# Performance work log

Measured on AMD Instinct MI355X. Metric: run time of the kernel, lower is better.

The kernel has to match this reference:

```python
import jax, jax.numpy as jnp
from jax import lax
import numpy as np

B = 16384
D = 32
N_HEADS = 4


def _piece_table():
    base = np.zeros((7, 4, 4), np.int32)
    cells = [
        [(1, 0), (1, 1), (1, 2), (1, 3)],  # I
        [(1, 1), (1, 2), (2, 1), (2, 2)],  # O
        [(1, 1), (2, 0), (2, 1), (2, 2)],  # T
        [(1, 1), (1, 2), (2, 0), (2, 1)],  # S
        [(1, 0), (1, 1), (2, 1), (2, 2)],  # Z
        [(1, 0), (2, 0), (2, 1), (2, 2)],  # J
        [(1, 2), (2, 0), (2, 1), (2, 2)],  # L
    ]
    for i, cs in enumerate(cells):
        for (r, c) in cs:
            base[i, r, c] = 1
    rots = np.stack([np.stack([np.rot90(base[i], k) for k in range(4)]) for i in range(7)])
    p = np.concatenate([rots, np.zeros((1, 4, 4, 4), np.int32)], 0)  # [8,4,4,4]
    return jnp.asarray(p)


def setup_inputs() -> dict:
    key = jax.random.key(0)
    ks = jax.random.split(key, 24)

    def ri(k, n, lo, hi):
        return jax.random.randint(k, (B, n), lo, hi, dtype=jnp.int32)

    t = jnp.concatenate([
        ri(ks[0], 1, 0, 10),   # col0 feature
        ri(ks[1], 1, 2, 8),
        ri(ks[2], 1, 0, 10),   # col2 y pos
        ri(ks[3], 1, 0, 8),    # col3 drop dist
        ri(ks[4], 1, 0, 4),    # col4 rotation
        ri(ks[5], 3, 0, 10),   # cols5-7
        ri(ks[6], 1, 0, 7),    # col8 piece id
        ri(ks[7], 6, 0, 7),    # cols9-14 hold/next
        ri(ks[8], 7, 0, 10),   # cols15-21
        ri(ks[9], 210, 0, 2),  # cols22-231 board
    ], axis=1)

    s = 0.05
    rn = lambda k, shp: jax.random.normal(k, shp, jnp.float32) * s
    return {
        "t": t,
        "piece_table": _piece_table(),
        "conv1_w": rn(ks[10], (6, 3, 5, 5)), "conv1_b": rn(ks[11], (6,)),
        "conv2_w": rn(ks[12], (16, 6, 5, 5)), "conv2_b": rn(ks[13], (16,)),
        "conv3_w": rn(ks[14], (64, 16, 3, 1)), "conv3_b": rn(ks[15], (64,)),
        "lfc1_w": rn(ks[16], (32, 64)), "lfc1_b": rn(ks[17], (32,)),
        "fc_w": rn(ks[18], (32, 8)), "fc_b": rn(ks[19], (32,)),
        "emb": rn(ks[20], (8, D)),
        "in_proj_w": rn(ks[21], (3 * D, D)), "in_proj_b": jnp.zeros((3 * D,), jnp.float32),
        "out_proj_w": rn(ks[22], (D, D)), "out_proj_b": jnp.zeros((D,), jnp.float32),
    }


def _avgpool2(x):
    b, c, h, w = x.shape
    h2, w2 = h // 2, w // 2
    return x[:, :, :h2 * 2, :w2 * 2].reshape(b, c, h2, 2, w2, 2).mean((3, 5))


def _lenet(x, w1, b1, w2, b2, w3, b3, fw, fb):
    dn = ("NCHW", "OIHW", "NCHW")
    x = jax.nn.relu(lax.conv_general_dilated(x, w1, (1, 1), ((2, 2), (2, 2)), dimension_numbers=dn) + b1[None, :, None, None])
    x = _avgpool2(x)                                   # [B,6,11,6]
    x = jax.nn.relu(lax.conv_general_dilated(x, w2, (1, 1), ((0, 0), (0, 0)), dimension_numbers=dn) + b2[None, :, None, None])
    x = _avgpool2(x)                                   # [B,16,3,1]
    x = jax.nn.relu(lax.conv_general_dilated(x, w3, (1, 1), ((0, 0), (0, 0)), dimension_numbers=dn) + b3[None, :, None, None])
    x = x.reshape(-1, 64)
    return jax.nn.relu(x @ fw.T + fb)                  # [B,32]


def _pe():
    pos = jnp.array([0, 0, 1, 2, 3, 4, 5], jnp.float32)[:, None]
    div = jnp.exp(jnp.arange(0, D, 2, dtype=jnp.float32) * (-jnp.log(10000.0) / D))
    s, c = jnp.sin(pos * div), jnp.cos(pos * div)      # [7,16] each
    return jnp.stack([s, c], -1).reshape(7, D)         # interleaved sin/cos


def _mha(q_in, kv, in_w, in_b, out_w, out_b):
    qw, kw, vw = in_w[:D], in_w[D:2 * D], in_w[2 * D:]
    qb, kb, vb = in_b[:D], in_b[D:2 * D], in_b[2 * D:]
    b, lq, _ = q_in.shape
    hd = D // N_HEADS
    q = (q_in @ qw.T + qb).reshape(b, lq, N_HEADS, hd)
    k = (kv @ kw.T + kb).reshape(b, -1, N_HEADS, hd)
    v = (kv @ vw.T + vb).reshape(b, -1, N_HEADS, hd)
    scores = jnp.einsum("bqhd,bkhd->bhqk", q, k) / jnp.sqrt(jnp.float32(hd))
    w = jax.nn.softmax(scores, axis=-1)
    o = jnp.einsum("bhqk,bkhd->bqhd", w, v).reshape(b, lq, D)
    return o @ out_w.T + out_b


def reference(t, piece_table, conv1_w, conv1_b, conv2_w, conv2_b, conv3_w, conv3_b,
              lfc1_w, lfc1_b, fc_w, fc_b, emb, in_proj_w, in_proj_b, out_proj_w, out_proj_b):
    bsz = t.shape[0]
    board = jnp.zeros((bsz, 3, 21, 10), jnp.float32)
    board = board.at[:, 0].set(t[:, 22:232].astype(jnp.float32).reshape(bsz, 21, 10))

    # gather piece grid, extract the 4 filled cells per sample in row-major order
    pieces = piece_table[t[:, 8], t[:, 4]].reshape(bsz, 16)        # [B,16] in {0,1}
    idx = jnp.argsort(1 - pieces, axis=1, stable=True)[:, :4]      # first 4 ones, scan order
    cy, cx = idx // 4, idx % 4
    x = cx + t[:, 1][:, None] - 2
    y = cy + t[:, 2][:, None]
    ny = y + t[:, 3][:, None]
    mask = (y >= 0) & (ny >= 0)
    br = jnp.arange(bsz, dtype=jnp.int32)[:, None]
    y_m = jnp.where(mask, y, -1)
    ny_m = jnp.where(mask, ny, -1)
    board = board.at[br, 1, y_m, x].set(1.0, mode="drop")
    board = board.at[br, 2, ny_m, x].set(1.0, mode="drop")

    board = jnp.pad(board, ((0, 0), (0, 0), (0, 1), (1, 1)), constant_values=1.0)  # [B,3,22,12]

    t9 = jnp.where((t[:, 9] != -1) & (t[:, 6] != 0), t[:, 9], 7)
    hold_next = jnp.concatenate([t[:, 8:9], t9[:, None], t[:, 10:15]], axis=1)     # [B,7]

    b2 = _lenet(board, conv1_w, conv1_b, conv2_w, conv2_b, conv3_w, conv3_b, lfc1_w, lfc1_b)  # [B,32]
    bkv = b2[:, None, :]                                            # [B,1,32]
    p = emb[hold_next] + _pe()[None]                                # [B,7,32]
    a = _mha(p, bkv, in_proj_w, in_proj_b, out_proj_w, out_proj_b)  # [B,7,32]

    xf = jax.nn.relu(t[:, :8].astype(jnp.float32) @ fc_w.T + fc_b)  # [B,32]
    out = jnp.concatenate([xf, a.mean(axis=1), b2], axis=1)         # [B,96]
    return (out, board)
```

## Files before the change

### kernel.cpp

```cpp
#include <hip/hip_runtime.h>
#include <cstddef>


#define BATCH 16384
#define SPB   4
#define NBLK  (BATCH / SPB)
#define RS    18
#define SBE_SZ 432
#define P1OFF  432
#define PCSOFF 800
#define SS2    816

__global__ __launch_bounds__(256)
void cborder_kernel(const float* __restrict__ w1, float* __restrict__ cb)
{
  int i = blockIdx.x * 256 + threadIdx.x;
  if (i >= 1584) return;
  int p = i / 6, o = i - p * 6;
  int y0 = p / 12, x0 = p - y0 * 12;
  float acc = 0.f;
#pragma unroll
  for (int dy = 0; dy < 5; ++dy)
#pragma unroll
    for (int dx = 0; dx < 5; ++dx) {
      int pr = y0 + dy - 2, pc = x0 + dx - 2;
      if (pr >= 0 && pr < 22 && pc >= 0 && pc < 12 &&
          (pr == 21 || pc == 0 || pc == 11)) {
        int k = dy * 5 + dx;
        acc += w1[(o * 3 + 0) * 25 + k] + w1[(o * 3 + 1) * 25 + k]
             + w1[(o * 3 + 2) * 25 + k];
      }
    }
  cb[p * 6 + o] = acc;
}

__global__ __launch_bounds__(256)
void board_model_kernel(const int* __restrict__ t,
                        const int* __restrict__ piece_table,
                        const float* __restrict__ w1, const float* __restrict__ b1,
                        const float* __restrict__ w2, const float* __restrict__ b2w,
                        const float* __restrict__ w3, const float* __restrict__ b3,
                        const float* __restrict__ wf1, const float* __restrict__ bf1,
                        const float* __restrict__ fcw, const float* __restrict__ fcb,
                        const float* __restrict__ ipw, const float* __restrict__ ipb,
                        const float* __restrict__ opw, const float* __restrict__ opb,
                        const float* __restrict__ cbg,
                        float* __restrict__ out,
                        float* __restrict__ out_board)
{
  __shared__ __align__(16) float scr[SPB * SS2];
  __shared__ float w1L[300];
  __shared__ float cbL[1440];

  const int tid  = threadIdx.x;
  const int lane = tid & 63;
  const int wv   = tid >> 6;
  const int bb   = blockIdx.x * SPB;

  for (int i = tid; i < 300; i += 256)
    w1L[i] = w1[(i / 50) * 75 + 25 + (i % 50)];
  for (int i = tid; i < 1440; i += 256) cbL[i] = cbg[i];

  {
    float* W = &scr[wv * SS2];
    int*   pcs = (int*)&scr[wv * SS2 + PCSOFF];
    const int* tr = t + (size_t)(bb + wv) * 232;

    float4* W4 = (float4*)W;
    for (int i = lane; i < 108; i += 64) W4[i] = float4{0.f, 0.f, 0.f, 0.f};

    for (int i = lane; i < 210; i += 64) {
      int r = i / 10, b = i - r * 10;
      W[(r + 2) * RS + b + 5] = (float)tr[22 + i];
    }

    if (lane < 4) {
      const int* pt = piece_table + (tr[8] * 4 + tr[4]) * 16;
      int sel = -1, n1 = 0;
#pragma unroll
      for (int j = 0; j < 16; ++j) { if (pt[j]) { if (n1 == lane) sel = j; ++n1; } }
      if (sel < 0) {
        int n0 = 0, want = lane - n1;
#pragma unroll
        for (int j = 0; j < 16; ++j) if (!pt[j]) { if (n0 == want) { sel = j; break; } ++n0; }
      }
      int cy = sel >> 2, cx = sel & 3;
      int x  = cx + tr[1] - 2;
      int y  = cy + tr[2];
      int ny = y + tr[3];
      bool mask = (y >= 0) && (ny >= 0);
      bool xok  = (x >= 0) && (x < 10);
      bool v1 = mask && xok && (y < 21);
      bool v2 = mask && xok && (ny < 21);
      pcs[2 * lane + 0]       = v1 ? y  : -100;
      pcs[2 * lane + 1]       = x + 1;
      pcs[2 * (lane + 4)]     = v2 ? ny : -100;
      pcs[2 * (lane + 4) + 1] = x + 1;
    }
    __builtin_amdgcn_wave_barrier();

    float* ob = out_board + (size_t)(bb + wv) * 792;
    for (int v = lane; v < 198; v += 64) {
      int j0 = v * 4;
      int ch = j0 / 264, rem = j0 - ch * 264;
      int r = rem / 12, c = rem - r * 12;
      float val[4];
      if (ch == 0) {
#pragma unroll
        for (int d = 0; d < 4; ++d) {
          int cd = c + d;
          val[d] = (r == 21 || cd == 0 || cd == 11) ? 1.f
                 : W[(r + 2) * RS + cd + 4];
        }
      } else {
#pragma unroll
        for (int d = 0; d < 4; ++d) {
          int cd = c + d;
          val[d] = (r == 21 || cd == 0 || cd == 11) ? 1.f : 0.f;
        }
#pragma unroll
        for (int e = 0; e < 4; ++e) {
          int pr = pcs[2 * ((ch - 1) * 4 + e)];
          int pc = pcs[2 * ((ch - 1) * 4 + e) + 1];
          if (pr == r && (unsigned)(pc - c) < 4u) val[pc - c] = 1.f;
        }
      }
      *(float4*)(ob + j0) = float4{val[0], val[1], val[2], val[3]};
    }
  }
  __syncthreads();

  if (lane < 60) {
    int p = lane;
    int r = p / 6, c = p - r * 6;
    const float* Wq  = &scr[wv * SS2];
    const int*   pcs = (const int*)&scr[wv * SS2 + PCSOFF];
    float acc[2][2][6];
#pragma unroll
    for (int i = 0; i < 2; ++i)
#pragma unroll
      for (int j = 0; j < 2; ++j) {
        int pcell = (2 * r + i) * 12 + (2 * c + j);
#pragma unroll
        for (int o = 0; o < 6; ++o)
          acc[i][j][o] = b1[o] + cbL[pcell * 6 + o];
      }

    {
      const float* base = Wq + (2 * r) * RS + (2 * c + 2);
#pragma unroll
      for (int u = 0; u < 6; ++u) {
        float2 a0 = *(const float2*)(base + u * RS);
        float2 a1 = *(const float2*)(base + u * RS + 2);
        float2 a2 = *(const float2*)(base + u * RS + 4);
        float rv[6] = {a0.x, a0.y, a1.x, a1.y, a2.x, a2.y};
#pragma unroll
        for (int i = 0; i < 2; ++i) {
          if (u - i < 0 || u - i > 4) continue;
          const int ky = u - i;
#pragma unroll
          for (int j = 0; j < 2; ++j)
#pragma unroll
            for (int kx = 0; kx < 5; ++kx) {
              float xv = rv[j + kx];
#pragma unroll
              for (int o = 0; o < 6; ++o)
                acc[i][j][o] += xv * w1[o * 75 + ky * 5 + kx];
            }
        }
      }
    }

#pragma unroll
    for (int e = 0; e < 8; ++e) {
      int pr = pcs[2 * e];
      if (pr < 0) continue;
      int pc = pcs[2 * e + 1];
      int chm = e >> 2;
      int dyb = pr + 2 - 2 * r;
      int dxb = pc + 2 - 2 * c;
      if (dyb < 0 || dyb > 5 || dxb < 0 || dxb > 5) continue;
#pragma unroll
      for (int i = 0; i < 2; ++i) {
        int dy = dyb - i;
        if ((unsigned)dy >= 5u) continue;
#pragma unroll
        for (int j = 0; j < 2; ++j) {
          int dx = dxb - j;
          if ((unsigned)dx >= 5u) continue;
#pragma unroll
          for (int o = 0; o < 6; ++o)
            acc[i][j][o] += w1L[(o * 2 + chm) * 25 + dy * 5 + dx];
        }
      }
    }

    float* P1q = &scr[wv * SS2 + P1OFF];
#pragma unroll
    for (int o = 0; o < 6; ++o) {
      float v = fmaxf(acc[0][0][o], 0.f) + fmaxf(acc[0][1][o], 0.f)
              + fmaxf(acc[1][0][o], 0.f) + fmaxf(acc[1][1][o], 0.f);
      P1q[o * 61 + p] = 0.25f * v;
    }
  }
  __syncthreads();

  const int wvu = __builtin_amdgcn_readfirstlane(wv);

  if (lane < 48) {
    int q = lane / 12, p = lane - q * 12;
    int r = p >> 1, c = p & 1;
    const float* P1q = &scr[q * SS2 + P1OFF];
    float a4[4];
#pragma unroll
    for (int oo = 0; oo < 4; ++oo) a4[oo] = b2w[4 * wvu + oo];
    for (int ic = 0; ic < 6; ++ic)
#pragma unroll
      for (int kr = 0; kr < 5; ++kr) {
        float xv[5];
#pragma unroll
        for (int kc = 0; kc < 5; ++kc)
          xv[kc] = P1q[ic * 61 + (r + kr) * 6 + c + kc];
#pragma unroll
        for (int kc = 0; kc < 5; ++kc)
#pragma unroll
          for (int oo = 0; oo < 4; ++oo)
            a4[oo] += xv[kc] * w2[(((4 * wvu + oo) * 6 + ic) * 5 + kr) * 5 + kc];
      }
    float* C2q = &scr[q * SS2];
#pragma unroll
    for (int oo = 0; oo < 4; ++oo)
      C2q[(4 * wvu + oo) * 12 + p] = fmaxf(a4[oo], 0.f);
  }
  __syncthreads();

  {
    const int q = wvu;
    float* S = &scr[q * SS2];

    if (lane < 48) {
      int o = lane / 3, pr = lane - o * 3;
      float v = 0.25f * (S[o * 12 + 4 * pr] + S[o * 12 + 4 * pr + 1]
                       + S[o * 12 + 4 * pr + 2] + S[o * 12 + 4 * pr + 3]);
      S[192 + lane] = v;
    }
    __builtin_amdgcn_wave_barrier();

    {
      int o = lane;
      float acc = b3[o];
#pragma unroll
      for (int k = 0; k < 48; ++k) acc += S[192 + k] * w3[o * 48 + k];
      S[240 + o] = fmaxf(acc, 0.f);
    }
    __builtin_amdgcn_wave_barrier();

    {
      int j = lane & 31, h = lane >> 5;
      float part = 0.f;
#pragma unroll
      for (int kk = 0; kk < 32; ++kk) {
        int k = 32 * h + kk;
        part += S[240 + k] * wf1[j * 64 + k];
      }
      part += __shfl_xor(part, 32, 64);
      if (h == 0) {
        float acc = fmaxf(bf1[j] + part, 0.f);
        S[304 + j] = acc;
        out[(size_t)(bb + q) * 96 + 64 + j] = acc;
      }
    }
    __builtin_amdgcn_wave_barrier();

    {
      int j = lane & 31;
      if (lane < 32) {
        float acc = ipb[64 + j];
#pragma unroll
        for (int k = 0; k < 32; ++k) acc += S[304 + k] * ipw[(64 + j) * 32 + k];
        S[336 + j] = acc;
      } else {
        const int* tr = t + (size_t)(bb + q) * 232;
        float acc = fcb[j];
#pragma unroll
        for (int k = 0; k < 8; ++k) acc += (float)tr[k] * fcw[j * 8 + k];
        out[(size_t)(bb + q) * 96 + j] = fmaxf(acc, 0.f);
      }
    }
    __builtin_amdgcn_wave_barrier();

    if (lane < 32) {
      int j = lane;
      float acc = opb[j];
#pragma unroll
      for (int k = 0; k < 32; ++k) acc += S[336 + k] * opw[j * 32 + k];
      out[(size_t)(bb + q) * 96 + 32 + j] = acc;
    }
  }
}

extern "C" void kernel_launch(void* const* d_in, const int* in_sizes, int n_in,
                              void* d_out, int out_size, void* d_ws, size_t ws_size,
                              hipStream_t stream) {
  const int*   t   = (const int*)d_in[0];
  const int*   pt  = (const int*)d_in[1];
  const float* w1  = (const float*)d_in[2];
  const float* b1  = (const float*)d_in[3];
  const float* w2  = (const float*)d_in[4];
  const float* b2w = (const float*)d_in[5];
  const float* w3  = (const float*)d_in[6];
  const float* b3  = (const float*)d_in[7];
  const float* wf1 = (const float*)d_in[8];
  const float* bf1 = (const float*)d_in[9];
  const float* fcw = (const float*)d_in[10];
  const float* fcb = (const float*)d_in[11];
  const float* ipw = (const float*)d_in[13];
  const float* ipb = (const float*)d_in[14];
  const float* opw = (const float*)d_in[15];
  const float* opb = (const float*)d_in[16];

  float* out       = (float*)d_out;
  float* out_board = out + (size_t)BATCH * 96;
  float* cbg       = (float*)d_ws;

  hipLaunchKernelGGL(cborder_kernel, dim3(7), dim3(256), 0, stream, w1, cbg);
  hipLaunchKernelGGL(board_model_kernel, dim3(NBLK), dim3(256), 0, stream,
                     t, pt, w1, b1, w2, b2w, w3, b3, wf1, bf1, fcw, fcb,
                     ipw, ipb, opw, opb, cbg, out, out_board);
}
```

Measured before the change: 196.3 us.

## Make each wave independent, drop block barriers, and repartition conv2 per wave

Every block-wide __syncthreads is replaced by wave-local fences and barriers, so each wave processes its own sample with no cross-wave dependency. conv2 is reassigned so each wave computes all 16 output channels for its own sample: 4 lanes per channel, 3 output rows each, with per-channel weights held in registers. The w1L shared staging is removed and the piece-cell conv1 terms now read w1 from global memory. Each wave also loads the whole cbL table itself, which adds redundant global traffic. The small dense layers use packed two-wide float vectors to encourage packed FMA instructions.

Result: slower. 219.5 us (+11.8%).

```diff
diff --git a/kernel.cpp b/kernel.cpp
--- a/kernel.cpp
+++ b/kernel.cpp
@@ -1,12 +1,13 @@
 #include <hip/hip_runtime.h>
 #include <cstddef>
 
+
+typedef float f32x2 __attribute__((ext_vector_type(2)));
 
 #define BATCH 16384
 #define SPB   4
 #define NBLK  (BATCH / SPB)
 #define RS    18
-#define SBE_SZ 432
 #define P1OFF  432
 #define PCSOFF 800
 #define SS2    816
@@ -31,7 +32,7 @@
              + w1[(o * 3 + 2) * 25 + k];
       }
     }
-  cb[p * 6 + o] = acc;
+  cb[i] = acc;
 }
 
 __global__ __launch_bounds__(256)
@@ -49,23 +50,20 @@
                         float* __restrict__ out_board)
 {
   __shared__ __align__(16) float scr[SPB * SS2];
-  __shared__ float w1L[300];
   __shared__ float cbL[1440];
 
   const int tid  = threadIdx.x;
   const int lane = tid & 63;
   const int wv   = tid >> 6;
-  const int bb   = blockIdx.x * SPB;
-
-  for (int i = tid; i < 300; i += 256)
-    w1L[i] = w1[(i / 50) * 75 + 25 + (i % 50)];
-  for (int i = tid; i < 1440; i += 256) cbL[i] = cbg[i];
+  const int s    = blockIdx.x * SPB + wv;
+
+  float* W   = &scr[wv * SS2];
+  int*   pcs = (int*)&scr[wv * SS2 + PCSOFF];
+  const int* tr = t + (size_t)s * 232;
+
+  for (int i = lane; i < 1440; i += 64) cbL[i] = cbg[i];
 
   {
-    float* W = &scr[wv * SS2];
-    int*   pcs = (int*)&scr[wv * SS2 + PCSOFF];
-    const int* tr = t + (size_t)(bb + wv) * 232;
-
     float4* W4 = (float4*)W;
     for (int i = lane; i < 108; i += 64) W4[i] = float4{0.f, 0.f, 0.f, 0.f};
 
@@ -97,9 +95,12 @@
       pcs[2 * (lane + 4)]     = v2 ? ny : -100;
       pcs[2 * (lane + 4) + 1] = x + 1;
     }
-    __builtin_amdgcn_wave_barrier();
-
-    float* ob = out_board + (size_t)(bb + wv) * 792;
+  }
+  __threadfence_block();
+  __builtin_amdgcn_wave_barrier();
+
+  {
+    float* ob = out_board + (size_t)s * 792;
     for (int v = lane; v < 198; v += 64) {
       int j0 = v * 4;
       int ch = j0 / 264, rem = j0 - ch * 264;
@@ -128,13 +129,10 @@
       *(float4*)(ob + j0) = float4{val[0], val[1], val[2], val[3]};
     }
   }
-  __syncthreads();
 
   if (lane < 60) {
     int p = lane;
     int r = p / 6, c = p - r * 6;
-    const float* Wq  = &scr[wv * SS2];
-    const int*   pcs = (const int*)&scr[wv * SS2 + PCSOFF];
     float acc[2][2][6];
 #pragma unroll
     for (int i = 0; i < 2; ++i)
@@ -147,7 +145,7 @@
       }
 
     {
-      const float* base = Wq + (2 * r) * RS + (2 * c + 2);
+      const float* base = W + (2 * r) * RS + (2 * c + 2);
 #pragma unroll
       for (int u = 0; u < 6; ++u) {
         float2 a0 = *(const float2*)(base + u * RS);
@@ -190,12 +188,12 @@
           if ((unsigned)dx >= 5u) continue;
 #pragma unroll
           for (int o = 0; o < 6; ++o)
-            acc[i][j][o] += w1L[(o * 2 + chm) * 25 + dy * 5 + dx];
-        }
-      }
-    }
-
-    float* P1q = &scr[wv * SS2 + P1OFF];
+            acc[i][j][o] += w1[(o * 3 + 1 + chm) * 25 + dy * 5 + dx];
+        }
+      }
+    }
+
+    float* P1q = W + P1OFF;
 #pragma unroll
     for (int o = 0; o < 6; ++o) {
       float v = fmaxf(acc[0][0][o], 0.f) + fmaxf(acc[0][1][o], 0.f)
@@ -203,40 +201,51 @@
       P1q[o * 61 + p] = 0.25f * v;
     }
   }
-  __syncthreads();
-
-  const int wvu = __builtin_amdgcn_readfirstlane(wv);
-
-  if (lane < 48) {
-    int q = lane / 12, p = lane - q * 12;
-    int r = p >> 1, c = p & 1;
-    const float* P1q = &scr[q * SS2 + P1OFF];
-    float a4[4];
-#pragma unroll
-    for (int oo = 0; oo < 4; ++oo) a4[oo] = b2w[4 * wvu + oo];
-    for (int ic = 0; ic < 6; ++ic)
-#pragma unroll
-      for (int kr = 0; kr < 5; ++kr) {
+  __threadfence_block();
+  __builtin_amdgcn_wave_barrier();
+
+  {
+    const int oc = lane >> 2;
+    const int pq = lane & 3;
+    const int r0 = pq >> 1, c0 = pq & 1;
+    const float* P1q = W + P1OFF;
+    float a3[3];
+    float bv = b2w[oc];
+    a3[0] = bv; a3[1] = bv; a3[2] = bv;
+    for (int ic = 0; ic < 6; ++ic) {
+      float wch[25];
+#pragma unroll
+      for (int j = 0; j < 25; ++j)
+        wch[j] = w2[oc * 150 + ic * 25 + j];
+#pragma unroll
+      for (int u = 0; u < 9; ++u) {
         float xv[5];
 #pragma unroll
         for (int kc = 0; kc < 5; ++kc)
-          xv[kc] = P1q[ic * 61 + (r + kr) * 6 + c + kc];
-#pragma unroll
-        for (int kc = 0; kc < 5; ++kc)
-#pragma unroll
-          for (int oo = 0; oo < 4; ++oo)
-            a4[oo] += xv[kc] * w2[(((4 * wvu + oo) * 6 + ic) * 5 + kr) * 5 + kc];
-      }
-    float* C2q = &scr[q * SS2];
-#pragma unroll
-    for (int oo = 0; oo < 4; ++oo)
-      C2q[(4 * wvu + oo) * 12 + p] = fmaxf(a4[oo], 0.f);
-  }
-  __syncthreads();
+          xv[kc] = P1q[ic * 61 + (r0 + u) * 6 + c0 + kc];
+        if (u <= 4) {
+#pragma unroll
+          for (int kc = 0; kc < 5; ++kc) a3[0] += xv[kc] * wch[u * 5 + kc];
+        }
+        if (u >= 2 && u <= 6) {
+#pragma unroll
+          for (int kc = 0; kc < 5; ++kc) a3[1] += xv[kc] * wch[(u - 2) * 5 + kc];
+        }
+        if (u >= 4) {
+#pragma unroll
+          for (int kc = 0; kc < 5; ++kc) a3[2] += xv[kc] * wch[(u - 4) * 5 + kc];
+        }
+      }
+    }
+    W[oc * 12 + pq]     = fmaxf(a3[0], 0.f);
+    W[oc * 12 + pq + 4] = fmaxf(a3[1], 0.f);
+    W[oc * 12 + pq + 8] = fmaxf(a3[2], 0.f);
+  }
+  __threadfence_block();
+  __builtin_amdgcn_wave_barrier();
 
   {
-    const int q = wvu;
-    float* S = &scr[q * SS2];
+    float* S = W;
 
     if (lane < 48) {
       int o = lane / 3, pr = lane - o * 3;
@@ -244,57 +253,70 @@
                        + S[o * 12 + 4 * pr + 2] + S[o * 12 + 4 * pr + 3]);
       S[192 + lane] = v;
     }
+    __threadfence_block();
     __builtin_amdgcn_wave_barrier();
 
     {
       int o = lane;
-      float acc = b3[o];
-#pragma unroll
-      for (int k = 0; k < 48; ++k) acc += S[192 + k] * w3[o * 48 + k];
-      S[240 + o] = fmaxf(acc, 0.f);
-    }
+      const f32x2* w3r = (const f32x2*)(w3 + o * 48);
+      f32x2 accp = f32x2{b3[o], 0.f};
+#pragma unroll
+      for (int k2 = 0; k2 < 24; ++k2)
+        accp += *(const f32x2*)(S + 192 + 2 * k2) * w3r[k2];
+      S[240 + o] = fmaxf(accp.x + accp.y, 0.f);
+    }
+    __threadfence_block();
     __builtin_amdgcn_wave_barrier();
 
     {
       int j = lane & 31, h = lane >> 5;
-      float part = 0.f;
-#pragma unroll
-      for (int kk = 0; kk < 32; ++kk) {
-        int k = 32 * h + kk;
-        part += S[240 + k] * wf1[j * 64 + k];
-      }
+      const f32x2* wr = (const f32x2*)(wf1 + j * 64 + 32 * h);
+      f32x2 accp = f32x2{0.f, 0.f};
+#pragma unroll
+      for (int k2 = 0; k2 < 16; ++k2)
+        accp += *(const f32x2*)(S + 240 + 32 * h + 2 * k2) * wr[k2];
+      float part = accp.x + accp.y;
       part += __shfl_xor(part, 32, 64);
       if (h == 0) {
         float acc = fmaxf(bf1[j] + part, 0.f);
         S[304 + j] = acc;
-        out[(size_t)(bb + q) * 96 + 64 + j] = acc;
-      }
-    }
+        out[(size_t)s * 96 + 64 + j] = acc;
+      }
+    }
+    __threadfence_block();
     __builtin_amdgcn_wave_barrier();
 
     {
       int j = lane & 31;
       if (lane < 32) {
-        float acc = ipb[64 + j];
-#pragma unroll
-        for (int k = 0; k < 32; ++k) acc += S[304 + k] * ipw[(64 + j) * 32 + k];
-        S[336 + j] = acc;
+        const f32x2* wr = (const f32x2*)(ipw + (64 + j) * 32);
+        f32x2 accp = f32x2{ipb[64 + j], 0.f};
+#pragma unroll
+        for (int k2 = 0; k2 < 16; ++k2)
+          accp += *(const f32x2*)(S + 304 + 2 * k2) * wr[k2];
+        S[336 + j] = accp.x + accp.y;
       } else {
-        const int* tr = t + (size_t)(bb + q) * 232;
-        float acc = fcb[j];
-#pragma unroll
-        for (int k = 0; k < 8; ++k) acc += (float)tr[k] * fcw[j * 8 + k];
-        out[(size_t)(bb + q) * 96 + j] = fmaxf(acc, 0.f);
-      }
-    }
+        const f32x2* wr = (const f32x2*)(fcw + j * 8);
+        f32x2 accp = f32x2{fcb[j], 0.f};
+#pragma unroll
+        for (int k2 = 0; k2 < 4; ++k2) {
+          f32x2 tv = f32x2{(float)tr[2 * k2], (float)tr[2 * k2 + 1]};
+          accp += tv * wr[k2];
+        }
+        out[(size_t)s * 96 + j] = fmaxf(accp.x + accp.y, 0.f);
+      }
+    }
+    __threadfence_block();
     __builtin_amdgcn_wave_barrier();
 
     if (lane < 32) {
       int j = lane;
-      float acc = opb[j];
-#pragma unroll
-      for (int k = 0; k < 32; ++k) acc += S[336 + k] * opw[j * 32 + k];
-      out[(size_t)(bb + q) * 96 + 32 + j] = acc;
+      const f32x2* wr = (const f32x2*)(opw + j * 32);
+      f32x2 accp = f32x2{opb[j], 0.f};
+#pragma unroll
+      for (int k2 = 0; k2 < 16; ++k2)
+        accp += *(const f32x2*)(S + 336 + 2 * k2) * wr[k2];
+      out[(size_t)s * 96 + 32 + j] = accp.x + accp.y;
     }
   }
 }
```
